# Optimization experiments

Measured on AMD Instinct MI355X. Metric: run time of the kernel, lower is better.

## Reference

```python
import jax, jax.numpy as jnp
import numpy as np
from jax import lax

M, G = 16, 4
INP = 256
OUP = 256
K = 3
EPS = 1e-5


def _weightnet(x, gap_vec, fc1_w, fc1_b, fc2_w, inp, oup, stride):
    # x: [B, inp, H, W], gap_vec: [B, 16]
    B, _, H, W = x.shape
    a = jax.nn.sigmoid(gap_vec @ fc1_w.T + fc1_b)          # [B, M*oup]
    groups = G * oup                                        # 1024
    out_pg = (oup * inp * K * K) // groups                  # 576
    in_pg = (M * oup) // groups                             # 4
    a = a.reshape(B, groups, in_pg)
    w2 = fc2_w.reshape(groups, out_pg, in_pg)
    # grouped 1x1 conv generating per-sample conv weights
    xw = jnp.einsum('bgi,goi->bgo', a, w2)                  # [B, groups, out_pg]
    xw = xw.reshape(B * oup, inp, K, K)                     # per-sample kernels
    xr = x.reshape(1, B * inp, H, W)
    out = lax.conv_general_dilated(
        xr, xw, (stride, stride), [(1, 1), (1, 1)],
        dimension_numbers=('NCHW', 'OIHW', 'NCHW'),
        feature_group_count=B)
    return out.reshape(B, oup, out.shape[2], out.shape[3])


def _bn(x, g, b, m, v):
    scale = (g / jnp.sqrt(v + EPS))[:, None, None]
    return (x - m[:, None, None]) * scale + b[:, None, None]


def setup_inputs() -> dict:
    key = jax.random.key(0)
    ks = jax.random.split(key, 20)
    d = {}
    d['x'] = jax.random.normal(ks[0], (32, 256, 56, 56), jnp.float32)
    d['reduce_w'] = jax.random.normal(ks[1], (16, 256), jnp.float32) * 0.05
    d['reduce_b'] = jax.random.normal(ks[2], (16,), jnp.float32) * 0.05
    d['w1_fc1_w'] = jax.random.normal(ks[3], (4096, 16), jnp.float32) * 0.05
    d['w1_fc1_b'] = jax.random.normal(ks[4], (4096,), jnp.float32) * 0.05
    d['w1_fc2_w'] = jax.random.normal(ks[5], (589824, 4), jnp.float32) * 0.05
    d['bn1_g'] = jax.random.uniform(ks[6], (256,), jnp.float32) + 0.5
    d['bn1_b'] = jax.random.normal(ks[7], (256,), jnp.float32) * 0.05
    d['bn1_m'] = jax.random.normal(ks[8], (256,), jnp.float32) * 0.05
    d['bn1_v'] = jax.random.uniform(ks[9], (256,), jnp.float32) + 0.5
    d['w2_fc1_w'] = jax.random.normal(ks[10], (4096, 16), jnp.float32) * 0.05
    d['w2_fc1_b'] = jax.random.normal(ks[11], (4096,), jnp.float32) * 0.05
    d['w2_fc2_w'] = jax.random.normal(ks[12], (589824, 4), jnp.float32) * 0.05
    d['bn2_g'] = jax.random.uniform(ks[13], (256,), jnp.float32) + 0.5
    d['bn2_b'] = jax.random.normal(ks[14], (256,), jnp.float32) * 0.05
    d['bn2_m'] = jax.random.normal(ks[15], (256,), jnp.float32) * 0.05
    d['bn2_v'] = jax.random.uniform(ks[16], (256,), jnp.float32) + 0.5
    return d


def reference(x, reduce_w, reduce_b, w1_fc1_w, w1_fc1_b, w1_fc2_w,
              bn1_g, bn1_b, bn1_m, bn1_v,
              w2_fc1_w, w2_fc1_b, w2_fc2_w,
              bn2_g, bn2_b, bn2_m, bn2_v):
    # global average pool -> reduce 1x1 conv
    gap = x.mean(axis=(2, 3))                       # [B, in_planes]
    gap = gap @ reduce_w.T + reduce_b               # [B, 16]
    out = _weightnet(x, gap, w1_fc1_w, w1_fc1_b, w1_fc2_w, INP, OUP, 1)
    out = jax.nn.relu(_bn(out, bn1_g, bn1_b, bn1_m, bn1_v))
    out = _weightnet(out, gap, w2_fc1_w, w2_fc1_b, w2_fc2_w, OUP, OUP, 1)
    out = _bn(out, bn2_g, bn2_b, bn2_m, bn2_v)
    out = out + x                                   # identity shortcut (stride=1, in==out)
    return jax.nn.relu(out)
```

## Files before the change

### kernel.cpp

```cpp
#include <hip/hip_runtime.h>

typedef short bf16x8 __attribute__((ext_vector_type(8)));
typedef float f32x4 __attribute__((ext_vector_type(4)));

#define EPSV 1e-5f
#define BNUM 32
#define CH 256
#define HW 3136
#define PXT 3684
#define NCHUNK 32
#define PERB_SHORTS (NCHUNK*PXT*8)
#define WB_PERB 589824

__device__ __forceinline__ unsigned short f2bf(float f) {
  unsigned int u = __float_as_uint(f);
  u += 0x7fffu + ((u >> 16) & 1u);
  return (unsigned short)(u >> 16);
}

__device__ __forceinline__ void gld16(const void* g, void* l) {
  __builtin_amdgcn_global_load_lds((const __attribute__((address_space(1))) void*)g,
                                   (__attribute__((address_space(3))) void*)l,
                                   16, 0, 0);
}

__global__ void k_gapc(const float* __restrict__ x, float* __restrict__ gapc) {
  int bc = blockIdx.x;
  const float4* p4 = (const float4*)(x + (size_t)bc * HW);
  int t = threadIdx.x;
  float s = 0.f;
  for (int i = t; i < 784; i += 256) {
    float4 v = p4[i];
    s += v.x + v.y + v.z + v.w;
  }
  for (int off = 32; off; off >>= 1) s += __shfl_down(s, off, 64);
  __shared__ float red[4];
  int lane = t & 63, wv = t >> 6;
  if (lane == 0) red[wv] = s;
  __syncthreads();
  if (t == 0) gapc[bc] = (red[0] + red[1] + red[2] + red[3]) * (1.f / 3136.f);
}

__global__ void k_gap16(const float* __restrict__ gapc, const float* __restrict__ rw,
                        const float* __restrict__ rb, float* __restrict__ g16) {
  int t = threadIdx.x;
  int b = t >> 4, j = t & 15;
  const float* gc = gapc + b * 256;
  const float* w = rw + j * 256;
  float s = rb[j];
  for (int c = 0; c < 256; ++c) s += gc[c] * w[c];
  g16[t] = s;
}

__global__ void k_act(const float* __restrict__ g16,
                      const float* __restrict__ w1w, const float* __restrict__ w1b,
                      const float* __restrict__ w2w, const float* __restrict__ w2b,
                      float* __restrict__ a1, float* __restrict__ a2) {
  int idx = blockIdx.x * 256 + threadIdx.x;
  int which = idx >> 17;
  int r = idx & 131071;
  int b = r >> 12, m = r & 4095;
  const float* w = (which ? w2w : w1w) + m * 16;
  float s = which ? w2b[m] : w1b[m];
  const float* g = g16 + b * 16;
#pragma unroll
  for (int j = 0; j < 16; ++j) s += g[j] * w[j];
  float out = 1.f / (1.f + __expf(-s));
  (which ? a2 : a1)[r] = out;
}

__global__ void k_zero(unsigned short* __restrict__ xp1, unsigned short* __restrict__ xp2) {
  int bc = blockIdx.x;
  int t = threadIdx.x;
  uint4 z = {0u, 0u, 0u, 0u};
  for (int wbuf = 0; wbuf < 2; ++wbuf) {
    unsigned short* base = (wbuf ? xp2 : xp1) + (size_t)bc * (PXT * 8);
    uint4* p = (uint4*)base;
    if (t < 123) p[t] = z;
    p[3370 + t] = z;
    if (t < 58) p[3626 + t] = z;
    if (t < 56) {
      int e = 64 + (t + 1) * 58 + 57;
      p[e] = z;
      p[e + 1] = z;
    }
  }
}

__global__ void k_xpad(const float* __restrict__ x, unsigned short* __restrict__ xp) {
  int y = blockIdx.x, ch = blockIdx.y, b = blockIdx.z;
  int l = threadIdx.x;
  if (l >= 56) return;
  const float* src = x + ((size_t)(b * 256 + ch * 8)) * HW + y * 56 + l;
  ushort4 lo, hi;
  lo.x = f2bf(src[0 * HW]); lo.y = f2bf(src[1 * HW]);
  lo.z = f2bf(src[2 * HW]); lo.w = f2bf(src[3 * HW]);
  hi.x = f2bf(src[4 * HW]); hi.y = f2bf(src[5 * HW]);
  hi.z = f2bf(src[6 * HW]); hi.w = f2bf(src[7 * HW]);
  unsigned short* dst = xp + ((size_t)(b * NCHUNK + ch)) * (PXT * 8)
                           + (size_t)(64 + (y + 1) * 58 + (l + 1)) * 8;
  *(ushort4*)dst = lo;
  *(ushort4*)(dst + 4) = hi;
}

__global__ void k_wgen(const float* __restrict__ a, const float4* __restrict__ w2,
                       unsigned short* __restrict__ wb) {
  int og = blockIdx.x & 63, bg = blockIdx.x >> 6;
  int t = threadIdx.x;
  for (int bi = 0; bi < 4; ++bi) {
    int b = bg * 4 + bi;
    const float* ab = a + b * 4096;
    unsigned short* wbb = wb + (size_t)b * WB_PERB;
    for (int it = 0; it < 36; ++it) {
      int wi = it * 256 + t;
      int oc_l = wi / 2304;
      int r = wi - oc_l * 2304;
      int ic = r / 9;
      int k9 = r - ic * 9;
      int kh = k9 / 3;
      int kw = k9 - kh * 3;
      int oc = og * 4 + oc_l;
      int g = oc * 4 + (ic >> 6);
      int o = (ic & 63) * 9 + k9;
      float4 w4 = w2[g * 576 + o];
      float4 a4 = *(const float4*)(ab + g * 4);
      float s = w4.x * a4.x + w4.y * a4.y + w4.z * a4.z + w4.w * a4.w;
      int s_ = ic >> 5, kc_ = (ic >> 3) & 3, icl = ic & 7;
      int ocg_ = oc >> 7, ocl_ = oc & 127;
      wbb[(size_t)((kh * 8 + s_) * 2 + ocg_) * 12288 + kc_ * 3072 + ocl_ * 24 + kw * 8 + icl]
          = f2bf(s);
    }
  }
}

__global__ __launch_bounds__(256, 2)
void k_conv(const unsigned short* __restrict__ xpad,
            const unsigned short* __restrict__ wbuf,
            const float* __restrict__ bgp, const float* __restrict__ bbp,
            const float* __restrict__ bmp, const float* __restrict__ bvp,
            const float* __restrict__ resid,
            unsigned short* __restrict__ outpad,
            float* __restrict__ outf,
            const int mode) {
  __shared__ unsigned short sW[2][12288];
  __shared__ unsigned short sX[2][8192];

  const int tid = threadIdx.x;
  const int lane = tid & 63;
  const int wv = tid >> 6;
  const int wocg = wv >> 1;
  const int wpxg = wv & 1;
  const int ocl = lane & 15;
  const int kc = lane >> 4;

  int rid = blockIdx.x;
  int xcd = rid & 7;
  int j = rid >> 3;
  int b = xcd + 8 * (j / 30);
  int slot = j % 30;
  int bocg = slot & 1;
  int p0 = 58 + (slot >> 1) * 224;

  const unsigned short* xb = xpad + (size_t)b * PERB_SHORTS + 64 * 8;
  const unsigned short* wbb = wbuf + (size_t)b * WB_PERB + bocg * 12288;

  f32x4 acc[4][7];
#pragma unroll
  for (int i = 0; i < 4; ++i)
#pragma unroll
    for (int k = 0; k < 7; ++k)
      acc[i][k] = (f32x4){0.f, 0.f, 0.f, 0.f};

  auto STAGE = [&](int s, int kh, int buf) {
    const unsigned short* wsrc = wbb + (size_t)(kh * 8 + s) * 24576;
#pragma unroll
    for (int i = 0; i < 6; ++i)
      gld16(wsrc + (wv * 3072 + i * 512 + lane * 8), &sW[buf][wv * 3072 + i * 512]);
    int q0 = p0 + kh * 58 - 59;
    const unsigned short* xs = xb + ((long)(s * 4 + wv) * PXT + q0) * 8;
#pragma unroll
    for (int i = 0; i < 4; ++i)
      gld16(xs + (i * 64 + lane) * 8, &sX[buf][wv * 2048 + i * 512]);
  };

  STAGE(0, 0, 0);
  int cur = 0;
  for (int t = 0; t < 24; ++t) {
    __syncthreads();
    if (t + 1 < 24) {
      int tn = t + 1;
      STAGE(tn / 3, tn % 3, cur ^ 1);
    }
#pragma unroll
    for (int kw = 0; kw < 3; ++kw) {
      bf16x8 af[4], bfr[7];
#pragma unroll
      for (int fm = 0; fm < 4; ++fm)
        af[fm] = *(const bf16x8*)&sW[cur][kc * 3072 + (wocg * 64 + fm * 16 + ocl) * 24 + kw * 8];
#pragma unroll
      for (int fn = 0; fn < 7; ++fn)
        bfr[fn] = *(const bf16x8*)&sX[cur][kc * 2048 + (wpxg * 112 + fn * 16 + ocl + kw) * 8];
#pragma unroll
      for (int fm = 0; fm < 4; ++fm)
#pragma unroll
        for (int fn = 0; fn < 7; ++fn)
          acc[fm][fn] = __builtin_amdgcn_mfma_f32_16x16x32_bf16(af[fm], bfr[fn], acc[fm][fn], 0, 0, 0);
    }
    cur ^= 1;
  }

  __syncthreads();
  float* scb = (float*)&sX[0][0];
  if (tid < 128) {
    int oc = bocg * 128 + tid;
    float sc = bgp[oc] * rsqrtf(bvp[oc] + EPSV);
    scb[tid] = sc;
    scb[128 + tid] = bbp[oc] - bmp[oc] * sc;
  }
  __syncthreads();

  const int dpb = wpxg * 112 + ocl;
  if (mode == 1) {
#pragma unroll
    for (int fn = 0; fn < 7; ++fn) {
      int pp = p0 + dpb + fn * 16;
      int py = pp / 58;
      int px = pp - py * 58;
      if (py < 1 || py > 56 || px < 1 || px > 56) continue;
#pragma unroll
      for (int fm = 0; fm < 4; ++fm) {
        int loc = wocg * 64 + fm * 16 + kc * 4;
        f32x4 v = acc[fm][fn];
        ushort4 w;
        w.x = f2bf(fmaxf(v[0] * scb[loc + 0] + scb[128 + loc + 0], 0.f));
        w.y = f2bf(fmaxf(v[1] * scb[loc + 1] + scb[128 + loc + 1], 0.f));
        w.z = f2bf(fmaxf(v[2] * scb[loc + 2] + scb[128 + loc + 2], 0.f));
        w.w = f2bf(fmaxf(v[3] * scb[loc + 3] + scb[128 + loc + 3], 0.f));
        int ocg_g = bocg * 128 + loc;
        *(ushort4*)&outpad[((size_t)(b * NCHUNK + (ocg_g >> 3))) * (PXT * 8)
                           + (size_t)(64 + pp) * 8 + (ocg_g & 7)] = w;
      }
    }
  } else {
#pragma unroll
    for (int fn = 0; fn < 7; ++fn) {
      int pp = p0 + dpb + fn * 16;
      int py = pp / 58;
      int px = pp - py * 58;
      if (py < 1 || py > 56 || px < 1 || px > 56) continue;
      int obase = (py - 1) * 56 + (px - 1);
#pragma unroll
      for (int fm = 0; fm < 4; ++fm) {
        int loc = wocg * 64 + fm * 16 + kc * 4;
        f32x4 v = acc[fm][fn];
#pragma unroll
        for (int r = 0; r < 4; ++r) {
          int oc = bocg * 128 + loc + r;
          size_t oi = ((size_t)(b * CH + oc)) * HW + obase;
          float tv = v[r] * scb[loc + r] + scb[128 + loc + r] + resid[oi];
          outf[oi] = fmaxf(tv, 0.f);
        }
      }
    }
  }
}

#define OFF_XP1 ((size_t)0)
#define XP_BYTES ((size_t)BNUM * PERB_SHORTS * 2)
#define OFF_XP2 (OFF_XP1 + XP_BYTES)
#define OFF_WB  (OFF_XP2 + XP_BYTES)
#define WB_BYTES ((size_t)BNUM * WB_PERB * 2)
#define OFF_GAPC (OFF_WB + WB_BYTES)
#define OFF_G16  (OFF_GAPC + 32768)
#define OFF_A1   (OFF_G16 + 2048)
#define OFF_A2   (OFF_A1 + 524288)

extern "C" void kernel_launch(void* const* d_in, const int* in_sizes, int n_in,
                              void* d_out, int out_size, void* d_ws, size_t ws_size,
                              hipStream_t stream) {
  (void)in_sizes; (void)n_in; (void)out_size; (void)ws_size;
  const float* x        = (const float*)d_in[0];
  const float* reduce_w = (const float*)d_in[1];
  const float* reduce_b = (const float*)d_in[2];
  const float* w1fc1w   = (const float*)d_in[3];
  const float* w1fc1b   = (const float*)d_in[4];
  const float* w1fc2w   = (const float*)d_in[5];
  const float* bn1g     = (const float*)d_in[6];
  const float* bn1b     = (const float*)d_in[7];
  const float* bn1m     = (const float*)d_in[8];
  const float* bn1v     = (const float*)d_in[9];
  const float* w2fc1w   = (const float*)d_in[10];
  const float* w2fc1b   = (const float*)d_in[11];
  const float* w2fc2w   = (const float*)d_in[12];
  const float* bn2g     = (const float*)d_in[13];
  const float* bn2b     = (const float*)d_in[14];
  const float* bn2m     = (const float*)d_in[15];
  const float* bn2v     = (const float*)d_in[16];

  char* ws = (char*)d_ws;
  unsigned short* xp1 = (unsigned short*)(ws + OFF_XP1);
  unsigned short* xp2 = (unsigned short*)(ws + OFF_XP2);
  unsigned short* wb  = (unsigned short*)(ws + OFF_WB);
  float* gapc = (float*)(ws + OFF_GAPC);
  float* g16  = (float*)(ws + OFF_G16);
  float* a1   = (float*)(ws + OFF_A1);
  float* a2   = (float*)(ws + OFF_A2);
  float* outf = (float*)d_out;

  k_gapc<<<BNUM * CH, 256, 0, stream>>>(x, gapc);
  k_gap16<<<1, 512, 0, stream>>>(gapc, reduce_w, reduce_b, g16);
  k_act<<<1024, 256, 0, stream>>>(g16, w1fc1w, w1fc1b, w2fc1w, w2fc1b, a1, a2);
  k_zero<<<1024, 256, 0, stream>>>(xp1, xp2);
  k_xpad<<<dim3(56, NCHUNK, BNUM), 64, 0, stream>>>(x, xp1);

  k_wgen<<<512, 256, 0, stream>>>(a1, (const float4*)w1fc2w, wb);
  k_conv<<<960, 256, 0, stream>>>(xp1, wb, bn1g, bn1b, bn1m, bn1v,
                                  nullptr, xp2, nullptr, 1);
  k_wgen<<<512, 256, 0, stream>>>(a2, (const float4*)w2fc2w, wb);
  k_conv<<<960, 256, 0, stream>>>(xp2, wb, bn2g, bn2b, bn2m, bn2v,
                                  x, nullptr, outf, 2);
}
```

Baseline: 430.7 us.

## Widen conv blocks to all 256 output channels with 512 threads and pipelined staging

The conv kernel now uses 512-thread blocks that each cover all 256 output channels for a pixel strip, so the input tile is loaded once per block instead of once per output-channel half. The weight layout from wgen changes to match the larger weight tile in LDS. The loop replaces __syncthreads with explicit vmcnt waits plus raw barriers so the next stage's loads stay in flight during compute, and it raises wave priority around the MFMA bursts. This adds LDS per block and reduces occupancy to one block of 8 waves, with a risk of wrong counts in the hand-written waitcnt.

```diff
diff --git a/kernel.cpp b/kernel.cpp
--- a/kernel.cpp
+++ b/kernel.cpp
@@ -125,15 +125,12 @@
       float4 w4 = w2[g * 576 + o];
       float4 a4 = *(const float4*)(ab + g * 4);
       float s = w4.x * a4.x + w4.y * a4.y + w4.z * a4.z + w4.w * a4.w;
-      int s_ = ic >> 5, kc_ = (ic >> 3) & 3, icl = ic & 7;
-      int ocg_ = oc >> 7, ocl_ = oc & 127;
-      wbb[(size_t)((kh * 8 + s_) * 2 + ocg_) * 12288 + kc_ * 3072 + ocl_ * 24 + kw * 8 + icl]
-          = f2bf(s);
-    }
-  }
-}
-
-__global__ __launch_bounds__(256, 2)
+      wbb[kh * 196608 + (ic >> 3) * 6144 + oc * 24 + kw * 8 + (ic & 7)] = f2bf(s);
+    }
+  }
+}
+
+__global__ __launch_bounds__(512, 1)
 void k_conv(const unsigned short* __restrict__ xpad,
             const unsigned short* __restrict__ wbuf,
             const float* __restrict__ bgp, const float* __restrict__ bbp,
@@ -142,7 +139,7 @@
             unsigned short* __restrict__ outpad,
             float* __restrict__ outf,
             const int mode) {
-  __shared__ unsigned short sW[2][12288];
+  __shared__ unsigned short sW[2][24576];
   __shared__ unsigned short sX[2][8192];
 
   const int tid = threadIdx.x;
@@ -156,13 +153,12 @@
   int rid = blockIdx.x;
   int xcd = rid & 7;
   int j = rid >> 3;
-  int b = xcd + 8 * (j / 30);
-  int slot = j % 30;
-  int bocg = slot & 1;
-  int p0 = 58 + (slot >> 1) * 224;
+  int b = xcd + 8 * (j / 15);
+  int slot = j % 15;
+  int p0 = 58 + slot * 224;
 
   const unsigned short* xb = xpad + (size_t)b * PERB_SHORTS + 64 * 8;
-  const unsigned short* wbb = wbuf + (size_t)b * WB_PERB + bocg * 12288;
+  const unsigned short* wbb = wbuf + (size_t)b * WB_PERB;
 
   f32x4 acc[4][7];
 #pragma unroll
@@ -171,51 +167,62 @@
     for (int k = 0; k < 7; ++k)
       acc[i][k] = (f32x4){0.f, 0.f, 0.f, 0.f};
 
-  auto STAGE = [&](int s, int kh, int buf) {
+  auto STAGE = [&](int t, int buf) {
+    int s = t >> 2;
+    s = t / 3;
+    int kh = t - s * 3;
     const unsigned short* wsrc = wbb + (size_t)(kh * 8 + s) * 24576;
 #pragma unroll
-    for (int i = 0; i < 6; ++i)
-      gld16(wsrc + (wv * 3072 + i * 512 + lane * 8), &sW[buf][wv * 3072 + i * 512]);
+    for (int i = 0; i < 6; ++i) {
+      int seg = wv * 6 + i;
+      gld16(wsrc + seg * 512 + lane * 8, &sW[buf][seg * 512]);
+    }
     int q0 = p0 + kh * 58 - 59;
-    const unsigned short* xs = xb + ((long)(s * 4 + wv) * PXT + q0) * 8;
-#pragma unroll
-    for (int i = 0; i < 4; ++i)
-      gld16(xs + (i * 64 + lane) * 8, &sX[buf][wv * 2048 + i * 512]);
+    int chunk = wv >> 1, half = wv & 1;
+    const unsigned short* xs = xb + ((long)(s * 4 + chunk) * PXT + q0 + half * 128) * 8;
+#pragma unroll
+    for (int i = 0; i < 2; ++i)
+      gld16(xs + (i * 64 + lane) * 8, &sX[buf][chunk * 2048 + half * 1024 + i * 512]);
   };
 
-  STAGE(0, 0, 0);
+  STAGE(0, 0);
   int cur = 0;
   for (int t = 0; t < 24; ++t) {
-    __syncthreads();
     if (t + 1 < 24) {
-      int tn = t + 1;
-      STAGE(tn / 3, tn % 3, cur ^ 1);
-    }
+      STAGE(t + 1, cur ^ 1);
+      asm volatile("s_waitcnt vmcnt(8)" ::: "memory");
+    } else {
+      asm volatile("s_waitcnt vmcnt(0)" ::: "memory");
+    }
+    __builtin_amdgcn_s_barrier();
+    __builtin_amdgcn_sched_barrier(0);
 #pragma unroll
     for (int kw = 0; kw < 3; ++kw) {
       bf16x8 af[4], bfr[7];
 #pragma unroll
       for (int fm = 0; fm < 4; ++fm)
-        af[fm] = *(const bf16x8*)&sW[cur][kc * 3072 + (wocg * 64 + fm * 16 + ocl) * 24 + kw * 8];
+        af[fm] = *(const bf16x8*)&sW[cur][kc * 6144 + (wocg * 64 + fm * 16 + ocl) * 24 + kw * 8];
 #pragma unroll
       for (int fn = 0; fn < 7; ++fn)
         bfr[fn] = *(const bf16x8*)&sX[cur][kc * 2048 + (wpxg * 112 + fn * 16 + ocl + kw) * 8];
+      __builtin_amdgcn_s_setprio(1);
 #pragma unroll
       for (int fm = 0; fm < 4; ++fm)
 #pragma unroll
         for (int fn = 0; fn < 7; ++fn)
           acc[fm][fn] = __builtin_amdgcn_mfma_f32_16x16x32_bf16(af[fm], bfr[fn], acc[fm][fn], 0, 0, 0);
-    }
+      __builtin_amdgcn_s_setprio(0);
+    }
+    __builtin_amdgcn_s_barrier();
     cur ^= 1;
   }
 
   __syncthreads();
   float* scb = (float*)&sX[0][0];
-  if (tid < 128) {
-    int oc = bocg * 128 + tid;
-    float sc = bgp[oc] * rsqrtf(bvp[oc] + EPSV);
+  if (tid < 256) {
+    float sc = bgp[tid] * rsqrtf(bvp[tid] + EPSV);
     scb[tid] = sc;
-    scb[128 + tid] = bbp[oc] - bmp[oc] * sc;
+    scb[256 + tid] = bbp[tid] - bmp[tid] * sc;
   }
   __syncthreads();
 
@@ -232,13 +239,12 @@
         int loc = wocg * 64 + fm * 16 + kc * 4;
         f32x4 v = acc[fm][fn];
         ushort4 w;
-        w.x = f2bf(fmaxf(v[0] * scb[loc + 0] + scb[128 + loc + 0], 0.f));
-        w.y = f2bf(fmaxf(v[1] * scb[loc + 1] + scb[128 + loc + 1], 0.f));
-        w.z = f2bf(fmaxf(v[2] * scb[loc + 2] + scb[128 + loc + 2], 0.f));
-        w.w = f2bf(fmaxf(v[3] * scb[loc + 3] + scb[128 + loc + 3], 0.f));
-        int ocg_g = bocg * 128 + loc;
-        *(ushort4*)&outpad[((size_t)(b * NCHUNK + (ocg_g >> 3))) * (PXT * 8)
-                           + (size_t)(64 + pp) * 8 + (ocg_g & 7)] = w;
+        w.x = f2bf(fmaxf(v[0] * scb[loc + 0] + scb[256 + loc + 0], 0.f));
+        w.y = f2bf(fmaxf(v[1] * scb[loc + 1] + scb[256 + loc + 1], 0.f));
+        w.z = f2bf(fmaxf(v[2] * scb[loc + 2] + scb[256 + loc + 2], 0.f));
+        w.w = f2bf(fmaxf(v[3] * scb[loc + 3] + scb[256 + loc + 3], 0.f));
+        *(ushort4*)&outpad[((size_t)(b * NCHUNK + (loc >> 3))) * (PXT * 8)
+                           + (size_t)(64 + pp) * 8 + (loc & 7)] = w;
       }
     }
   } else {
@@ -255,9 +261,9 @@
         f32x4 v = acc[fm][fn];
 #pragma unroll
         for (int r = 0; r < 4; ++r) {
-          int oc = bocg * 128 + loc + r;
+          int oc = loc + r;
           size_t oi = ((size_t)(b * CH + oc)) * HW + obase;
-          float tv = v[r] * scb[loc + r] + scb[128 + loc + r] + resid[oi];
+          float tv = v[r] * scb[oc] + scb[256 + oc] + resid[oi];
           outf[oi] = fmaxf(tv, 0.f);
         }
       }
@@ -314,9 +320,9 @@
   k_xpad<<<dim3(56, NCHUNK, BNUM), 64, 0, stream>>>(x, xp1);
 
   k_wgen<<<512, 256, 0, stream>>>(a1, (const float4*)w1fc2w, wb);
-  k_conv<<<960, 256, 0, stream>>>(xp1, wb, bn1g, bn1b, bn1m, bn1v,
+  k_conv<<<480, 512, 0, stream>>>(xp1, wb, bn1g, bn1b, bn1m, bn1v,
                                   nullptr, xp2, nullptr, 1);
   k_wgen<<<512, 256, 0, stream>>>(a2, (const float4*)w2fc2w, wb);
-  k_conv<<<960, 256, 0, stream>>>(xp2, wb, bn2g, bn2b, bn2m, bn2v,
+  k_conv<<<480, 512, 0, stream>>>(xp2, wb, bn2g, bn2b, bn2m, bn2v,
                                   x, nullptr, outf, 2);
 }
```

Result: slower. 466.3 us (+8.3%).

## Load conv activations directly into registers and parallelize gap reduction

Applied to the files above, without the earlier changes.

The conv kernel no longer stages activation tiles through LDS. Each wave loads its B fragments straight from global memory into registers, software-pipelined across kw phases with a manual vmcnt wait, and MFMA issue priority is raised via setprio. This halves LDS traffic and frees LDS, at the risk of redundant global loads, higher register pressure and a fragile hand-set waitcnt. Separately, the tiny 16-dim reduce GEMV is spread over 32 blocks with a shuffle reduction instead of one block of serial loops.

```diff
diff --git a/kernel.cpp b/kernel.cpp
--- a/kernel.cpp
+++ b/kernel.cpp
@@ -43,13 +43,17 @@
 
 __global__ void k_gap16(const float* __restrict__ gapc, const float* __restrict__ rw,
                         const float* __restrict__ rb, float* __restrict__ g16) {
+  int b = blockIdx.x;
   int t = threadIdx.x;
-  int b = t >> 4, j = t & 15;
+  int j = t >> 5;
+  int c0 = t & 31;
   const float* gc = gapc + b * 256;
   const float* w = rw + j * 256;
-  float s = rb[j];
-  for (int c = 0; c < 256; ++c) s += gc[c] * w[c];
-  g16[t] = s;
+  float s = 0.f;
+#pragma unroll
+  for (int k = 0; k < 8; ++k) s += gc[c0 + k * 32] * w[c0 + k * 32];
+  for (int off = 16; off; off >>= 1) s += __shfl_down(s, off, 32);
+  if (c0 == 0) g16[b * 16 + j] = s + rb[j];
 }
 
 __global__ void k_act(const float* __restrict__ g16,
@@ -143,7 +147,7 @@
             float* __restrict__ outf,
             const int mode) {
   __shared__ unsigned short sW[2][12288];
-  __shared__ unsigned short sX[2][8192];
+  __shared__ float scb[256];
 
   const int tid = threadIdx.x;
   const int lane = tid & 63;
@@ -171,46 +175,57 @@
     for (int k = 0; k < 7; ++k)
       acc[i][k] = (f32x4){0.f, 0.f, 0.f, 0.f};
 
-  auto STAGE = [&](int s, int kh, int buf) {
+  auto STAGE_W = [&](int t, int buf) {
+    int s = t / 3;
+    int kh = t - s * 3;
     const unsigned short* wsrc = wbb + (size_t)(kh * 8 + s) * 24576;
 #pragma unroll
-    for (int i = 0; i < 6; ++i)
-      gld16(wsrc + (wv * 3072 + i * 512 + lane * 8), &sW[buf][wv * 3072 + i * 512]);
-    int q0 = p0 + kh * 58 - 59;
-    const unsigned short* xs = xb + ((long)(s * 4 + wv) * PXT + q0) * 8;
-#pragma unroll
-    for (int i = 0; i < 4; ++i)
-      gld16(xs + (i * 64 + lane) * 8, &sX[buf][wv * 2048 + i * 512]);
+    for (int i = 0; i < 6; ++i) {
+      int seg = wv * 6 + i;
+      gld16(wsrc + seg * 512 + lane * 8, &sW[buf][seg * 512]);
+    }
   };
-
-  STAGE(0, 0, 0);
+  auto XLOAD = [&](bf16x8 (&bx)[7], int t, int kw) {
+    int s = t / 3;
+    int kh = t - s * 3;
+    const bf16x8* xr = (const bf16x8*)(xb +
+        ((long)(s * 4 + kc) * PXT + p0 + kh * 58 - 59 + wpxg * 112 + ocl + kw) * 8);
+#pragma unroll
+    for (int fn = 0; fn < 7; ++fn) bx[fn] = xr[fn * 16];
+  };
+  auto PHASE = [&](bf16x8 (&bx)[7], int cur, int kw) {
+    bf16x8 af[4];
+#pragma unroll
+    for (int fm = 0; fm < 4; ++fm)
+      af[fm] = *(const bf16x8*)&sW[cur][kc * 3072 + (wocg * 64 + fm * 16 + ocl) * 24 + kw * 8];
+    __builtin_amdgcn_s_setprio(1);
+#pragma unroll
+    for (int fm = 0; fm < 4; ++fm)
+#pragma unroll
+      for (int fn = 0; fn < 7; ++fn)
+        acc[fm][fn] = __builtin_amdgcn_mfma_f32_16x16x32_bf16(af[fm], bx[fn], acc[fm][fn], 0, 0, 0);
+    __builtin_amdgcn_s_setprio(0);
+  };
+
+  bf16x8 bx0[7], bx1[7], bx2[7];
+
+  STAGE_W(0, 0);
+  XLOAD(bx0, 0, 0);
+
   int cur = 0;
   for (int t = 0; t < 24; ++t) {
-    __syncthreads();
-    if (t + 1 < 24) {
-      int tn = t + 1;
-      STAGE(tn / 3, tn % 3, cur ^ 1);
-    }
-#pragma unroll
-    for (int kw = 0; kw < 3; ++kw) {
-      bf16x8 af[4], bfr[7];
-#pragma unroll
-      for (int fm = 0; fm < 4; ++fm)
-        af[fm] = *(const bf16x8*)&sW[cur][kc * 3072 + (wocg * 64 + fm * 16 + ocl) * 24 + kw * 8];
-#pragma unroll
-      for (int fn = 0; fn < 7; ++fn)
-        bfr[fn] = *(const bf16x8*)&sX[cur][kc * 2048 + (wpxg * 112 + fn * 16 + ocl + kw) * 8];
-#pragma unroll
-      for (int fm = 0; fm < 4; ++fm)
-#pragma unroll
-        for (int fn = 0; fn < 7; ++fn)
-          acc[fm][fn] = __builtin_amdgcn_mfma_f32_16x16x32_bf16(af[fm], bfr[fn], acc[fm][fn], 0, 0, 0);
-    }
+    asm volatile("s_waitcnt vmcnt(7)" ::: "memory");
+    __builtin_amdgcn_s_barrier();
+    if (t + 1 < 24) STAGE_W(t + 1, cur ^ 1);
+    XLOAD(bx1, t, 1);
+    XLOAD(bx2, t, 2);
+    PHASE(bx0, cur, 0);
+    PHASE(bx1, cur, 1);
+    if (t + 1 < 24) XLOAD(bx0, t + 1, 0);
+    PHASE(bx2, cur, 2);
     cur ^= 1;
   }
 
-  __syncthreads();
-  float* scb = (float*)&sX[0][0];
   if (tid < 128) {
     int oc = bocg * 128 + tid;
     float sc = bgp[oc] * rsqrtf(bvp[oc] + EPSV);
@@ -308,7 +323,7 @@
   float* outf = (float*)d_out;
 
   k_gapc<<<BNUM * CH, 256, 0, stream>>>(x, gapc);
-  k_gap16<<<1, 512, 0, stream>>>(gapc, reduce_w, reduce_b, g16);
+  k_gap16<<<BNUM, 512, 0, stream>>>(gapc, reduce_w, reduce_b, g16);
   k_act<<<1024, 256, 0, stream>>>(g16, w1fc1w, w1fc1b, w2fc1w, w2fc1b, a1, a2);
   k_zero<<<1024, 256, 0, stream>>>(xp1, xp2);
   k_xpad<<<dim3(56, NCHUNK, BNUM), 64, 0, stream>>>(x, xp1);
```

New measurement: 451.9 us. +4.9%, slower.
